# Kernel optimization log

Hardware: AMD Instinct MI355X
Metric: run time of the kernel (lower is better)

## Reference

```python
import jax, jax.numpy as jnp
import numpy as np


def _gru(x, w_ih, w_hh, b_ih, b_hh):
    # x: [B, T, D]; torch nn.GRU (batch_first) semantics, h0 = 0
    B = x.shape[0]
    H = w_hh.shape[1]
    def step(h, xt):
        gi = xt @ w_ih.T + b_ih          # [B, 3H]
        gh = h @ w_hh.T + b_hh           # [B, 3H]
        ir, iz, inn = jnp.split(gi, 3, axis=-1)
        hr, hz, hn = jnp.split(gh, 3, axis=-1)
        r = jax.nn.sigmoid(ir + hr)
        z = jax.nn.sigmoid(iz + hz)
        n = jnp.tanh(inn + r * hn)
        h_new = (1.0 - z) * n + z * h
        return h_new, h_new
    h0 = jnp.zeros((B, H), x.dtype)
    _, ys = jax.lax.scan(step, h0, jnp.swapaxes(x, 0, 1))
    return jnp.swapaxes(ys, 0, 1)        # [B, T, H]


def setup_inputs() -> dict:
    key = jax.random.key(0)
    ks = iter(jax.random.split(key, 40))
    def p(shape, scale=0.05):
        return jax.random.normal(next(ks), shape, dtype=jnp.float32) * scale
    B, T, Z, S = 1024, 2, 100, 6
    return {
        "x": p((B, T, Z, S), 1.0),
        # actor: GRU(6 -> 64) + SimpleSubActor(64 -> 512 -> 128 -> 1)
        "a_gru_wih": p((192, 6)), "a_gru_whh": p((192, 64)),
        "a_gru_bih": p((192,)), "a_gru_bhh": p((192,)),
        "a_fc1_w": p((512, 64)), "a_fc1_b": p((512,)),
        "a_fc2_w": p((128, 512)), "a_fc2_b": p((128,)),
        "a_fc3_w": p((1, 128)), "a_fc3_b": p((1,)),
        # critic: GRU(35 -> 32) + SimpleSubCritic(32 -> 512 -> 256 -> 1)
        "c_gru_wih": p((96, 35)), "c_gru_whh": p((96, 32)),
        "c_gru_bih": p((96,)), "c_gru_bhh": p((96,)),
        "c_fc1_w": p((512, 32)), "c_fc1_b": p((512,)),
        "c_fc2_w": p((256, 512)), "c_fc2_b": p((256,)),
        "c_fc3_w": p((1, 256)), "c_fc3_b": p((1,)),
        # LocalizedModule(35 -> 512 -> 256 -> 1)
        "lm_fc1_w": p((512, 35)), "lm_fc1_b": p((512,)),
        "lm_fc2_w": p((256, 512)), "lm_fc2_b": p((256,)),
        "lm_fc3_w": p((1, 256)), "lm_fc3_b": p((1,)),
    }


def reference(x, a_gru_wih, a_gru_whh, a_gru_bih, a_gru_bhh,
              a_fc1_w, a_fc1_b, a_fc2_w, a_fc2_b, a_fc3_w, a_fc3_b,
              c_gru_wih, c_gru_whh, c_gru_bih, c_gru_bhh,
              c_fc1_w, c_fc1_b, c_fc2_w, c_fc2_b, c_fc3_w, c_fc3_b,
              lm_fc1_w, lm_fc1_b, lm_fc2_w, lm_fc2_b, lm_fc3_w, lm_fc3_b):
    B, T, Z, S = x.shape
    # ---- SimpleActor: same GRU+MLP shared across zones -> batch zones ----
    # torch: a[i] from x[:, :, i]; torch.stack(a) -> [Z, B, T, 1], then .view(-1, T, Z)
    xz = jnp.transpose(x, (2, 0, 1, 3)).reshape(Z * B, T, S)   # zones-major
    sx = _gru(xz, a_gru_wih, a_gru_whh, a_gru_bih, a_gru_bhh)  # [Z*B, T, 64]
    h = jax.nn.relu(sx @ a_fc1_w.T + a_fc1_b)
    h = jax.nn.relu(h @ a_fc2_w.T + a_fc2_b)
    sa = h @ a_fc3_w.T + a_fc3_b                               # [Z*B, T, 1]
    p = sa.reshape(-1, T, Z)                                   # faithful view(-1, t, nzones)
    # ---- concat action onto state ----
    xc = jnp.concatenate([x, p.reshape(-1, T, Z, 1)], axis=-1)  # [B, T, Z, 7]
    # ---- SimpleCritic: f/q lists reset each iter -> only zone i=99 survives ----
    # neighbors of 99: (99, 89, 100->zeros, 109->zeros, 98)
    zeros = jnp.zeros_like(xc[:, :, Z - 1])
    xi = jnp.concatenate([xc[:, :, 99], xc[:, :, 89], zeros, zeros, xc[:, :, 98]], axis=2)  # [B, T, 35]
    # LocalizedModule on last timestep
    hf = jax.nn.relu(xi[:, -1, :] @ lm_fc1_w.T + lm_fc1_b)
    hf = jax.nn.relu(hf @ lm_fc2_w.T + lm_fc2_b)
    f = hf @ lm_fc3_w.T + lm_fc3_b                             # [B, 1]
    # critic GRU + SimpleSubCritic (it keeps only last timestep)
    xq = _gru(xi, c_gru_wih, c_gru_whh, c_gru_bih, c_gru_bhh)  # [B, T, 32]
    hq = jax.nn.relu(xq[:, -1, :] @ c_fc1_w.T + c_fc1_b)
    hq = jax.nn.relu(hq @ c_fc2_w.T + c_fc2_b)
    qz = hq @ c_fc3_w.T + c_fc3_b                              # [B, 1]
    q = jnp.sum(f + qz, axis=1)                                # [B]
    return p[:, -1], q.reshape(-1, 1)
```

## Files before the change

### kernel.cpp

```cpp
#include <hip/hip_runtime.h>
#include <hip/hip_bf16.h>

#define NB 1024
#define NT 2
#define NZ 100
#define NS 6
#define NSEQ (NZ*NB)

typedef short short8 __attribute__((ext_vector_type(8)));
typedef float floatx4 __attribute__((ext_vector_type(4)));
typedef unsigned int uint2v __attribute__((ext_vector_type(2)));

__device__ __forceinline__ float sigm(float v)     { return 1.0f/(1.0f + __expf(-v)); }
__device__ __forceinline__ float tanhfast(float v) { float t = __expf(2.0f*v); return 1.0f - 2.0f/(t + 1.0f); }
__device__ __forceinline__ unsigned short f2bf(float f) {
    __hip_bfloat16 h = __float2bfloat16(f);
    return *reinterpret_cast<unsigned short*>(&h);
}
__device__ __forceinline__ float bf2f(unsigned short u) {
    __hip_bfloat16 h; *reinterpret_cast<unsigned short*>(&h) = u;
    return __bfloat162float(h);
}

#define WS_WIHB   819200
#define WS_WHHB   (WS_WIHB + 192*32*2)
#define WS_W1B    (WS_WHHB + 192*64*2)
#define WS_W2B    (WS_W1B + 512*64*2)
#define WS_L1WB   (WS_W2B + 128*512*2)
#define WS_L2WB   (WS_L1WB + 512*64*2)
#define WS_CF1WB  (WS_L2WB + 256*512*2)
#define WS_CF2WB  (WS_CF1WB + 512*32*2)
#define WS_CWIHB  (WS_CF2WB + 256*512*2)
#define WS_CWHHB  (WS_CWIHB + 96*64*2)

#define PREP_N (116736 + 32768 + 131072 + 16384 + 131072 + 6144 + 3072)

__global__ __launch_bounds__(256)
void prep_kernel(const float* __restrict__ wih, const float* __restrict__ whh,
                 const float* __restrict__ w1,  const float* __restrict__ w2,
                 const float* __restrict__ l1w, const float* __restrict__ l2w,
                 const float* __restrict__ cf1w, const float* __restrict__ cf2w,
                 const float* __restrict__ cwih, const float* __restrict__ cwhh,
                 unsigned short* wihb, unsigned short* whhb,
                 unsigned short* w1b,  unsigned short* w2b,
                 unsigned short* l1wb, unsigned short* l2wb,
                 unsigned short* cf1wb, unsigned short* cf2wb,
                 unsigned short* cwihb, unsigned short* cwhhb)
{
    int e = blockIdx.x*256 + threadIdx.x;
    if (e < 6144) {
        int g = e >> 5, k = e & 31;
        wihb[e] = f2bf(k < 6 ? wih[g*6 + k] : 0.0f);
    } else if (e < 18432) {
        int i = e - 6144;  whhb[i] = f2bf(whh[i]);
    } else if (e < 51200) {
        int i = e - 18432; w1b[i] = f2bf(w1[i]);
    } else if (e < 116736) {
        int i = e - 51200; w2b[i] = f2bf(w2[i]);
    } else if (e < 149504) {
        int i = e - 116736; int o = i >> 6, k = i & 63;
        l1wb[i] = f2bf(k < 35 ? l1w[o*35 + k] : 0.0f);
    } else if (e < 280576) {
        int i = e - 149504; l2wb[i] = f2bf(l2w[i]);
    } else if (e < 296960) {
        int i = e - 280576; cf1wb[i] = f2bf(cf1w[i]);
    } else if (e < 428032) {
        int i = e - 296960; cf2wb[i] = f2bf(cf2w[i]);
    } else if (e < 434176) {
        int i = e - 428032; int o = i >> 6, k = i & 63;
        cwihb[i] = f2bf(k < 35 ? cwih[o*35 + k] : 0.0f);
    } else if (e < PREP_N) {
        int i = e - 434176; cwhhb[i] = f2bf(cwhh[i]);
    }
}

__device__ __forceinline__ short8 ldsfrag(const char* base, int rowstride, int r, int k0) {
    int byte = r*rowstride + k0*2;
    byte ^= ((r & 7) << 4);
    return *reinterpret_cast<const short8*>(base + byte);
}

__global__ __launch_bounds__(512, 4)
void actor_mfma(const float* __restrict__ x,
                const unsigned short* __restrict__ wihb, const unsigned short* __restrict__ whhb,
                const float* __restrict__ bih, const float* __restrict__ bhh,
                const unsigned short* __restrict__ w1b, const float* __restrict__ b1,
                const unsigned short* __restrict__ w2b, const float* __restrict__ b2,
                const float* __restrict__ w3, const float* __restrict__ b3,
                float* __restrict__ sa, float* __restrict__ out0)
{
    __shared__ __align__(16) char smem[73728];
    char*  sxb  = smem;
    float* fc3p = (float*)smem;
    char*  h1b  = smem + 8192;
    char*  xpad = smem + 8192;
    char*  h0b  = smem + 24576;

    const int tid  = threadIdx.x;
    const int wv   = tid >> 6;
    const int lane = tid & 63;
    const int r16  = lane & 15;
    const int g4   = lane >> 4;
    const int ft   = wv & 3;
    const int sq   = wv >> 2;
    const int s0   = blockIdx.x * 32;
    const int zz   = s0 >> 10;
    const int b0   = s0 & 1023;

    for (int e = tid; e < 1024; e += 512) {
        int row = e >> 4, j = e & 15;
        int t = row >> 5, sl = row & 31;
        unsigned int lo = 0, hi = 0;
        if (j < 2) {
            const float* xp = x + (((b0 + sl)*NT + t)*NZ + zz)*NS;
            int c0 = j*4;
            float v0 = xp[c0], v1 = xp[c0+1];
            float v2 = (c0+2 < 6) ? xp[c0+2] : 0.0f;
            float v3 = (c0+3 < 6) ? xp[c0+3] : 0.0f;
            lo = (unsigned int)f2bf(v0) | ((unsigned int)f2bf(v1) << 16);
            hi = (unsigned int)f2bf(v2) | ((unsigned int)f2bf(v3) << 16);
        }
        int byte = row*128 + j*8; byte ^= ((row & 7) << 4);
        uint2v vv = {lo, hi};
        *reinterpret_cast<uint2v*>(xpad + byte) = vv;
    }

    const int fb = ft*16 + g4*4;
    const floatx4 bihR = *reinterpret_cast<const floatx4*>(bih + fb);
    const floatx4 bihZ = *reinterpret_cast<const floatx4*>(bih + 64 + fb);
    const floatx4 bihN = *reinterpret_cast<const floatx4*>(bih + 128 + fb);
    const floatx4 bhhR = *reinterpret_cast<const floatx4*>(bhh + fb);
    const floatx4 bhhZ = *reinterpret_cast<const floatx4*>(bhh + 64 + fb);
    const floatx4 bhhN = *reinterpret_cast<const floatx4*>(bhh + 128 + fb);
    __syncthreads();

    floatx4 h0;
    {
        short8 bx = ldsfrag(xpad, 128, sq*16 + r16, g4*8);
        const short8 aR = *reinterpret_cast<const short8*>(wihb + ((ft     )*16 + r16)*32 + g4*8);
        const short8 aZ = *reinterpret_cast<const short8*>(wihb + ((ft +  4)*16 + r16)*32 + g4*8);
        const short8 aN = *reinterpret_cast<const short8*>(wihb + ((ft +  8)*16 + r16)*32 + g4*8);
        floatx4 gR = {0,0,0,0}, gZ = {0,0,0,0}, gN = {0,0,0,0};
        gR = __builtin_amdgcn_mfma_f32_16x16x32_bf16(aR, bx, gR, 0, 0, 0);
        gZ = __builtin_amdgcn_mfma_f32_16x16x32_bf16(aZ, bx, gZ, 0, 0, 0);
        gN = __builtin_amdgcn_mfma_f32_16x16x32_bf16(aN, bx, gN, 0, 0, 0);
        #pragma unroll
        for (int q = 0; q < 4; ++q) {
            float r = sigm(gR[q] + bihR[q] + bhhR[q]);
            float z = sigm(gZ[q] + bihZ[q] + bhhZ[q]);
            float n = tanhfast(gN[q] + bihN[q] + r*bhhN[q]);
            h0[q] = (1.0f - z)*n;
        }
        unsigned int lo = (unsigned int)f2bf(h0[0]) | ((unsigned int)f2bf(h0[1]) << 16);
        unsigned int hi = (unsigned int)f2bf(h0[2]) | ((unsigned int)f2bf(h0[3]) << 16);
        uint2v vv = {lo, hi};
        int seq = sq*16 + r16;
        int b1a = seq*128 + fb*2; b1a ^= ((seq & 7) << 4);
        *reinterpret_cast<uint2v*>(h0b + b1a) = vv;
        *reinterpret_cast<uint2v*>(sxb + b1a) = vv;
    }

    floatx4 gR1 = {0,0,0,0}, gZ1 = {0,0,0,0}, gN1 = {0,0,0,0};
    {
        short8 bx = ldsfrag(xpad, 128, 32 + sq*16 + r16, g4*8);
        const short8 aR = *reinterpret_cast<const short8*>(wihb + ((ft     )*16 + r16)*32 + g4*8);
        const short8 aZ = *reinterpret_cast<const short8*>(wihb + ((ft +  4)*16 + r16)*32 + g4*8);
        const short8 aN = *reinterpret_cast<const short8*>(wihb + ((ft +  8)*16 + r16)*32 + g4*8);
        gR1 = __builtin_amdgcn_mfma_f32_16x16x32_bf16(aR, bx, gR1, 0, 0, 0);
        gZ1 = __builtin_amdgcn_mfma_f32_16x16x32_bf16(aZ, bx, gZ1, 0, 0, 0);
        gN1 = __builtin_amdgcn_mfma_f32_16x16x32_bf16(aN, bx, gN1, 0, 0, 0);
    }
    __syncthreads();

    {
        short8 bh0 = ldsfrag(h0b, 128, sq*16 + r16, g4*8);
        short8 bh1 = ldsfrag(h0b, 128, sq*16 + r16, 32 + g4*8);
        floatx4 hR = {0,0,0,0}, hZ = {0,0,0,0}, hN = {0,0,0,0};
        #pragma unroll
        for (int p = 0; p < 2; ++p) {
            short8 bh = p ? bh1 : bh0;
            const short8 aR = *reinterpret_cast<const short8*>(whhb + ((ft     )*16 + r16)*64 + p*32 + g4*8);
            const short8 aZ = *reinterpret_cast<const short8*>(whhb + ((ft +  4)*16 + r16)*64 + p*32 + g4*8);
            const short8 aN = *reinterpret_cast<const short8*>(whhb + ((ft +  8)*16 + r16)*64 + p*32 + g4*8);
            hR = __builtin_amdgcn_mfma_f32_16x16x32_bf16(aR, bh, hR, 0, 0, 0);
            hZ = __builtin_amdgcn_mfma_f32_16x16x32_bf16(aZ, bh, hZ, 0, 0, 0);
            hN = __builtin_amdgcn_mfma_f32_16x16x32_bf16(aN, bh, hN, 0, 0, 0);
        }
        floatx4 hn;
        #pragma unroll
        for (int q = 0; q < 4; ++q) {
            float r = sigm(gR1[q] + bihR[q] + hR[q] + bhhR[q]);
            float z = sigm(gZ1[q] + bihZ[q] + hZ[q] + bhhZ[q]);
            float n = tanhfast(gN1[q] + bihN[q] + r*(hN[q] + bhhN[q]));
            hn[q] = (1.0f - z)*n + z*h0[q];
        }
        unsigned int lo = (unsigned int)f2bf(hn[0]) | ((unsigned int)f2bf(hn[1]) << 16);
        unsigned int hi = (unsigned int)f2bf(hn[2]) | ((unsigned int)f2bf(hn[3]) << 16);
        uint2v vv = {lo, hi};
        int row = 32 + sq*16 + r16;
        int ba = row*128 + fb*2; ba ^= ((row & 7) << 4);
        *reinterpret_cast<uint2v*>(sxb + ba) = vv;
    }
    __syncthreads();

    {
        short8 bf[4][2];
        #pragma unroll
        for (int rt = 0; rt < 4; ++rt) {
            bf[rt][0] = ldsfrag(sxb, 128, rt*16 + r16, g4*8);
            bf[rt][1] = ldsfrag(sxb, 128, rt*16 + r16, 32 + g4*8);
        }
        #pragma unroll
        for (int j = 0; j < 4; ++j) {
            int mt = wv*4 + j;
            const short8 a0 = *reinterpret_cast<const short8*>(w1b + (mt*16 + r16)*64 + g4*8);
            const short8 a1 = *reinterpret_cast<const short8*>(w1b + (mt*16 + r16)*64 + 32 + g4*8);
            const floatx4 bias = *reinterpret_cast<const floatx4*>(b1 + mt*16 + g4*4);
            #pragma unroll
            for (int rt = 0; rt < 4; ++rt) {
                floatx4 acc = bias;
                acc = __builtin_amdgcn_mfma_f32_16x16x32_bf16(a0, bf[rt][0], acc, 0, 0, 0);
                acc = __builtin_amdgcn_mfma_f32_16x16x32_bf16(a1, bf[rt][1], acc, 0, 0, 0);
                unsigned int lo = (unsigned int)f2bf(fmaxf(acc[0],0.f)) | ((unsigned int)f2bf(fmaxf(acc[1],0.f)) << 16);
                unsigned int hi = (unsigned int)f2bf(fmaxf(acc[2],0.f)) | ((unsigned int)f2bf(fmaxf(acc[3],0.f)) << 16);
                int row = rt*16 + r16;
                int byte = row*1024 + (mt*16 + g4*4)*2; byte ^= ((row & 7) << 4);
                uint2v vv = {lo, hi};
                *reinterpret_cast<uint2v*>(h1b + byte) = vv;
            }
        }
    }
    __syncthreads();

    {
        floatx4 acc[4];
        const floatx4 bias = *reinterpret_cast<const floatx4*>(b2 + wv*16 + g4*4);
        #pragma unroll
        for (int rt = 0; rt < 4; ++rt) acc[rt] = bias;
        const unsigned short* wp = w2b + (wv*16 + r16)*512 + g4*8;
        for (int ks = 0; ks < 16; ++ks) {
            const short8 a = *reinterpret_cast<const short8*>(wp + ks*32);
            #pragma unroll
            for (int rt = 0; rt < 4; ++rt) {
                short8 bb = ldsfrag(h1b, 1024, rt*16 + r16, ks*32 + g4*8);
                acc[rt] = __builtin_amdgcn_mfma_f32_16x16x32_bf16(a, bb, acc[rt], 0, 0, 0);
            }
        }
        const floatx4 w3v = *reinterpret_cast<const floatx4*>(w3 + wv*16 + g4*4);
        #pragma unroll
        for (int rt = 0; rt < 4; ++rt) {
            float p = fmaxf(acc[rt][0],0.f)*w3v[0] + fmaxf(acc[rt][1],0.f)*w3v[1]
                    + fmaxf(acc[rt][2],0.f)*w3v[2] + fmaxf(acc[rt][3],0.f)*w3v[3];
            p += __shfl_xor(p, 16);
            p += __shfl_xor(p, 32);
            if (g4 == 0) fc3p[wv*64 + rt*16 + r16] = p;
        }
    }
    __syncthreads();

    if (tid < 64) {
        float v = b3[0];
        #pragma unroll
        for (int w = 0; w < 8; ++w) v += fc3p[w*64 + tid];
        int t = tid >> 5, sl = tid & 31;
        int gseq = s0 + sl;
        int i = gseq*2 + t;
        sa[i] = v;
        int m = i % 200;
        if (m >= 100) out0[(i/200)*NZ + (m - 100)] = v;
    }
}

__global__ __launch_bounds__(512)
void critic_mfma(const float* __restrict__ x, const float* __restrict__ sa,
                 const unsigned short* __restrict__ cwihb, const unsigned short* __restrict__ cwhhb,
                 const float* __restrict__ cbih, const float* __restrict__ cbhh,
                 const unsigned short* __restrict__ cf1wb, const float* __restrict__ cf1b,
                 const unsigned short* __restrict__ cf2wb, const float* __restrict__ cf2b,
                 const float* __restrict__ cf3w, const float* __restrict__ cf3b,
                 const unsigned short* __restrict__ l1wb, const float* __restrict__ l1b,
                 const unsigned short* __restrict__ l2wb, const float* __restrict__ l2b,
                 const float* __restrict__ l3w, const float* __restrict__ l3b,
                 float* __restrict__ outq)
{
    __shared__ __align__(16) char smem[25600];
    char*  xib = smem;
    char*  h1b = smem + 4096;
    char*  h0b = smem + 20480;
    char*  hqb = smem + 22528;
    float* fp  = (float*)(smem + 24576);
    float* qp  = (float*)(smem + 25088);

    const int tid  = threadIdx.x;
    const int wv   = tid >> 6;
    const int lane = tid & 63;
    const int r16  = lane & 15;
    const int g4   = lane >> 4;
    const int b0   = blockIdx.x * 16;

    for (int e = tid; e < 2048; e += 512) {
        int trow = e >> 6, k = e & 63;
        int t = trow >> 4, row = trow & 15;
        int b = b0 + row;
        float v = 0.0f;
        if (k < 35) {
            int slot = k / 7, s = k - slot*7;
            int nb = (slot==0)?99:((slot==1)?89:((slot==4)?98:-1));
            if (nb >= 0) v = (s < 6) ? x[((b*NT + t)*NZ + nb)*NS + s]
                                     : sa[b*200 + t*100 + nb];
        }
        int byte = trow*128 + k*2; byte ^= ((trow & 7) << 4);
        *reinterpret_cast<unsigned short*>(xib + byte) = f2bf(v);
    }
    __syncthreads();

    {
        short8 bx0 = ldsfrag(xib, 128, 16 + r16, g4*8);
        short8 bx1 = ldsfrag(xib, 128, 16 + r16, 32 + g4*8);
        #pragma unroll
        for (int j = 0; j < 4; ++j) {
            int mt = wv*4 + j;
            const short8 a0 = *reinterpret_cast<const short8*>(l1wb + (mt*16 + r16)*64 + g4*8);
            const short8 a1 = *reinterpret_cast<const short8*>(l1wb + (mt*16 + r16)*64 + 32 + g4*8);
            floatx4 acc = *reinterpret_cast<const floatx4*>(l1b + mt*16 + g4*4);
            acc = __builtin_amdgcn_mfma_f32_16x16x32_bf16(a0, bx0, acc, 0, 0, 0);
            acc = __builtin_amdgcn_mfma_f32_16x16x32_bf16(a1, bx1, acc, 0, 0, 0);
            unsigned int lo = (unsigned int)f2bf(fmaxf(acc[0],0.f)) | ((unsigned int)f2bf(fmaxf(acc[1],0.f)) << 16);
            unsigned int hi = (unsigned int)f2bf(fmaxf(acc[2],0.f)) | ((unsigned int)f2bf(fmaxf(acc[3],0.f)) << 16);
            int byte = r16*1024 + (mt*16 + g4*4)*2; byte ^= ((r16 & 7) << 4);
            uint2v vv = {lo, hi};
            *reinterpret_cast<uint2v*>(h1b + byte) = vv;
        }
    }
    __syncthreads();

    {
        int mt0 = wv*2, mt1 = wv*2 + 1;
        floatx4 acc0 = *reinterpret_cast<const floatx4*>(l2b + mt0*16 + g4*4);
        floatx4 acc1 = *reinterpret_cast<const floatx4*>(l2b + mt1*16 + g4*4);
        const unsigned short* wp0 = l2wb + (mt0*16 + r16)*512 + g4*8;
        const unsigned short* wp1 = l2wb + (mt1*16 + r16)*512 + g4*8;
        for (int ks = 0; ks < 16; ++ks) {
            short8 bb = ldsfrag(h1b, 1024, r16, ks*32 + g4*8);
            const short8 a0 = *reinterpret_cast<const short8*>(wp0 + ks*32);
            const short8 a1 = *reinterpret_cast<const short8*>(wp1 + ks*32);
            acc0 = __builtin_amdgcn_mfma_f32_16x16x32_bf16(a0, bb, acc0, 0, 0, 0);
            acc1 = __builtin_amdgcn_mfma_f32_16x16x32_bf16(a1, bb, acc1, 0, 0, 0);
        }
        const floatx4 w0 = *reinterpret_cast<const floatx4*>(l3w + mt0*16 + g4*4);
        const floatx4 w1 = *reinterpret_cast<const floatx4*>(l3w + mt1*16 + g4*4);
        float p = fmaxf(acc0[0],0.f)*w0[0] + fmaxf(acc0[1],0.f)*w0[1]
                + fmaxf(acc0[2],0.f)*w0[2] + fmaxf(acc0[3],0.f)*w0[3]
                + fmaxf(acc1[0],0.f)*w1[0] + fmaxf(acc1[1],0.f)*w1[1]
                + fmaxf(acc1[2],0.f)*w1[2] + fmaxf(acc1[3],0.f)*w1[3];
        p += __shfl_xor(p, 16);
        p += __shfl_xor(p, 32);
        if (g4 == 0) fp[wv*16 + r16] = p;
    }
    __syncthreads();

    floatx4 h0r = {0,0,0,0};
    floatx4 gR1 = {0,0,0,0}, gZ1 = {0,0,0,0}, gN1 = {0,0,0,0};
    floatx4 bihR, bihZ, bihN, bhhR, bhhZ, bhhN;
    if (wv < 2) {
        const int hf = wv;
        const int fb = hf*16 + g4*4;
        bihR = *reinterpret_cast<const floatx4*>(cbih + fb);
        bihZ = *reinterpret_cast<const floatx4*>(cbih + 32 + fb);
        bihN = *reinterpret_cast<const floatx4*>(cbih + 64 + fb);
        bhhR = *reinterpret_cast<const floatx4*>(cbhh + fb);
        bhhZ = *reinterpret_cast<const floatx4*>(cbhh + 32 + fb);
        bhhN = *reinterpret_cast<const floatx4*>(cbhh + 64 + fb);
        short8 bx0 = ldsfrag(xib, 128, r16, g4*8);
        short8 bx1 = ldsfrag(xib, 128, r16, 32 + g4*8);
        short8 cx0 = ldsfrag(xib, 128, 16 + r16, g4*8);
        short8 cx1 = ldsfrag(xib, 128, 16 + r16, 32 + g4*8);
        floatx4 gR0 = {0,0,0,0}, gZ0 = {0,0,0,0}, gN0 = {0,0,0,0};
        #pragma unroll
        for (int p = 0; p < 2; ++p) {
            const short8 aR = *reinterpret_cast<const short8*>(cwihb + ((hf    )*16 + r16)*64 + p*32 + g4*8);
            const short8 aZ = *reinterpret_cast<const short8*>(cwihb + ((2+hf  )*16 + r16)*64 + p*32 + g4*8);
            const short8 aN = *reinterpret_cast<const short8*>(cwihb + ((4+hf  )*16 + r16)*64 + p*32 + g4*8);
            short8 b0f = p ? bx1 : bx0;
            short8 b1f = p ? cx1 : cx0;
            gR0 = __builtin_amdgcn_mfma_f32_16x16x32_bf16(aR, b0f, gR0, 0, 0, 0);
            gZ0 = __builtin_amdgcn_mfma_f32_16x16x32_bf16(aZ, b0f, gZ0, 0, 0, 0);
            gN0 = __builtin_amdgcn_mfma_f32_16x16x32_bf16(aN, b0f, gN0, 0, 0, 0);
            gR1 = __builtin_amdgcn_mfma_f32_16x16x32_bf16(aR, b1f, gR1, 0, 0, 0);
            gZ1 = __builtin_amdgcn_mfma_f32_16x16x32_bf16(aZ, b1f, gZ1, 0, 0, 0);
            gN1 = __builtin_amdgcn_mfma_f32_16x16x32_bf16(aN, b1f, gN1, 0, 0, 0);
        }
        #pragma unroll
        for (int q = 0; q < 4; ++q) {
            float r = sigm(gR0[q] + bihR[q] + bhhR[q]);
            float z = sigm(gZ0[q] + bihZ[q] + bhhZ[q]);
            float n = tanhfast(gN0[q] + bihN[q] + r*bhhN[q]);
            h0r[q] = (1.0f - z)*n;
        }
        unsigned int lo = (unsigned int)f2bf(h0r[0]) | ((unsigned int)f2bf(h0r[1]) << 16);
        unsigned int hi = (unsigned int)f2bf(h0r[2]) | ((unsigned int)f2bf(h0r[3]) << 16);
        uint2v vv = {lo, hi};
        int byte = r16*128 + fb*2; byte ^= ((r16 & 7) << 4);
        *reinterpret_cast<uint2v*>(h0b + byte) = vv;
    }
    __syncthreads();
    if (wv < 2) {
        const int hf = wv;
        const int fb = hf*16 + g4*4;
        short8 bh = ldsfrag(h0b, 128, r16, g4*8);
        const short8 aR = *reinterpret_cast<const short8*>(cwhhb + ((hf    )*16 + r16)*32 + g4*8);
        const short8 aZ = *reinterpret_cast<const short8*>(cwhhb + ((2+hf  )*16 + r16)*32 + g4*8);
        const short8 aN = *reinterpret_cast<const short8*>(cwhhb + ((4+hf  )*16 + r16)*32 + g4*8);
        floatx4 hR = {0,0,0,0}, hZ = {0,0,0,0}, hN = {0,0,0,0};
        hR = __builtin_amdgcn_mfma_f32_16x16x32_bf16(aR, bh, hR, 0, 0, 0);
        hZ = __builtin_amdgcn_mfma_f32_16x16x32_bf16(aZ, bh, hZ, 0, 0, 0);
        hN = __builtin_amdgcn_mfma_f32_16x16x32_bf16(aN, bh, hN, 0, 0, 0);
        floatx4 hn;
        #pragma unroll
        for (int q = 0; q < 4; ++q) {
            float r = sigm(gR1[q] + bihR[q] + hR[q] + bhhR[q]);
            float z = sigm(gZ1[q] + bihZ[q] + hZ[q] + bhhZ[q]);
            float n = tanhfast(gN1[q] + bihN[q] + r*(hN[q] + bhhN[q]));
            hn[q] = (1.0f - z)*n + z*h0r[q];
        }
        unsigned int lo = (unsigned int)f2bf(hn[0]) | ((unsigned int)f2bf(hn[1]) << 16);
        unsigned int hi = (unsigned int)f2bf(hn[2]) | ((unsigned int)f2bf(hn[3]) << 16);
        uint2v vv = {lo, hi};
        int byte = r16*128 + fb*2; byte ^= ((r16 & 7) << 4);
        *reinterpret_cast<uint2v*>(hqb + byte) = vv;
    }
    __syncthreads();

    {
        short8 bq = ldsfrag(hqb, 128, r16, g4*8);
        #pragma unroll
        for (int j = 0; j < 4; ++j) {
            int mt = wv*4 + j;
            const short8 a = *reinterpret_cast<const short8*>(cf1wb + (mt*16 + r16)*32 + g4*8);
            floatx4 acc = *reinterpret_cast<const floatx4*>(cf1b + mt*16 + g4*4);
            acc = __builtin_amdgcn_mfma_f32_16x16x32_bf16(a, bq, acc, 0, 0, 0);
            unsigned int lo = (unsigned int)f2bf(fmaxf(acc[0],0.f)) | ((unsigned int)f2bf(fmaxf(acc[1],0.f)) << 16);
            unsigned int hi = (unsigned int)f2bf(fmaxf(acc[2],0.f)) | ((unsigned int)f2bf(fmaxf(acc[3],0.f)) << 16);
            int byte = r16*1024 + (mt*16 + g4*4)*2; byte ^= ((r16 & 7) << 4);
            uint2v vv = {lo, hi};
            *reinterpret_cast<uint2v*>(h1b + byte) = vv;
        }
    }
    __syncthreads();

    {
        int mt0 = wv*2, mt1 = wv*2 + 1;
        floatx4 acc0 = *reinterpret_cast<const floatx4*>(cf2b + mt0*16 + g4*4);
        floatx4 acc1 = *reinterpret_cast<const floatx4*>(cf2b + mt1*16 + g4*4);
        const unsigned short* wp0 = cf2wb + (mt0*16 + r16)*512 + g4*8;
        const unsigned short* wp1 = cf2wb + (mt1*16 + r16)*512 + g4*8;
        for (int ks = 0; ks < 16; ++ks) {
            short8 bb = ldsfrag(h1b, 1024, r16, ks*32 + g4*8);
            const short8 a0 = *reinterpret_cast<const short8*>(wp0 + ks*32);
            const short8 a1 = *reinterpret_cast<const short8*>(wp1 + ks*32);
            acc0 = __builtin_amdgcn_mfma_f32_16x16x32_bf16(a0, bb, acc0, 0, 0, 0);
            acc1 = __builtin_amdgcn_mfma_f32_16x16x32_bf16(a1, bb, acc1, 0, 0, 0);
        }
        const floatx4 w0 = *reinterpret_cast<const floatx4*>(cf3w + mt0*16 + g4*4);
        const floatx4 w1 = *reinterpret_cast<const floatx4*>(cf3w + mt1*16 + g4*4);
        float p = fmaxf(acc0[0],0.f)*w0[0] + fmaxf(acc0[1],0.f)*w0[1]
                + fmaxf(acc0[2],0.f)*w0[2] + fmaxf(acc0[3],0.f)*w0[3]
                + fmaxf(acc1[0],0.f)*w1[0] + fmaxf(acc1[1],0.f)*w1[1]
                + fmaxf(acc1[2],0.f)*w1[2] + fmaxf(acc1[3],0.f)*w1[3];
        p += __shfl_xor(p, 16);
        p += __shfl_xor(p, 32);
        if (g4 == 0) qp[wv*16 + r16] = p;
    }
    __syncthreads();

    if (tid < 16) {
        float f = l3b[0], qz = cf3b[0];
        #pragma unroll
        for (int w = 0; w < 8; ++w) { f += fp[w*16 + tid]; qz += qp[w*16 + tid]; }
        outq[b0 + tid] = f + qz;
    }
}

extern "C" void kernel_launch(void* const* d_in, const int* in_sizes, int n_in,
                              void* d_out, int out_size, void* d_ws, size_t ws_size,
                              hipStream_t stream)
{
    (void)in_sizes; (void)n_in; (void)out_size; (void)ws_size;
    const float* x     = (const float*)d_in[0];
    const float* a_wih = (const float*)d_in[1];
    const float* a_whh = (const float*)d_in[2];
    const float* a_bih = (const float*)d_in[3];
    const float* a_bhh = (const float*)d_in[4];
    const float* a1w   = (const float*)d_in[5];
    const float* a1b   = (const float*)d_in[6];
    const float* a2w   = (const float*)d_in[7];
    const float* a2b   = (const float*)d_in[8];
    const float* a3w   = (const float*)d_in[9];
    const float* a3b   = (const float*)d_in[10];
    const float* cwih  = (const float*)d_in[11];
    const float* cwhh  = (const float*)d_in[12];
    const float* cbih  = (const float*)d_in[13];
    const float* cbhh  = (const float*)d_in[14];
    const float* cf1w  = (const float*)d_in[15];
    const float* cf1b  = (const float*)d_in[16];
    const float* cf2w  = (const float*)d_in[17];
    const float* cf2b  = (const float*)d_in[18];
    const float* cf3w  = (const float*)d_in[19];
    const float* cf3b  = (const float*)d_in[20];
    const float* l1w   = (const float*)d_in[21];
    const float* l1b   = (const float*)d_in[22];
    const float* l2w   = (const float*)d_in[23];
    const float* l2b   = (const float*)d_in[24];
    const float* l3w   = (const float*)d_in[25];
    const float* l3b   = (const float*)d_in[26];

    float* sa = (float*)d_ws;
    unsigned short* wihb  = (unsigned short*)((char*)d_ws + WS_WIHB);
    unsigned short* whhb  = (unsigned short*)((char*)d_ws + WS_WHHB);
    unsigned short* w1b   = (unsigned short*)((char*)d_ws + WS_W1B);
    unsigned short* w2b   = (unsigned short*)((char*)d_ws + WS_W2B);
    unsigned short* l1wb  = (unsigned short*)((char*)d_ws + WS_L1WB);
    unsigned short* l2wb  = (unsigned short*)((char*)d_ws + WS_L2WB);
    unsigned short* cf1wb = (unsigned short*)((char*)d_ws + WS_CF1WB);
    unsigned short* cf2wb = (unsigned short*)((char*)d_ws + WS_CF2WB);
    unsigned short* cwihb = (unsigned short*)((char*)d_ws + WS_CWIHB);
    unsigned short* cwhhb = (unsigned short*)((char*)d_ws + WS_CWHHB);
    float* out0 = (float*)d_out;
    float* outq = (float*)d_out + NB*NZ;

    hipLaunchKernelGGL(prep_kernel, dim3((PREP_N + 255)/256), dim3(256), 0, stream,
                       a_wih, a_whh, a1w, a2w, l1w, l2w, cf1w, cf2w, cwih, cwhh,
                       wihb, whhb, w1b, w2b, l1wb, l2wb, cf1wb, cf2wb, cwihb, cwhhb);
    hipLaunchKernelGGL(actor_mfma, dim3(NSEQ/32), dim3(512), 0, stream,
                       x, wihb, whhb, a_bih, a_bhh, w1b, a1b, w2b, a2b, a3w, a3b, sa, out0);
    hipLaunchKernelGGL(critic_mfma, dim3(NB/16), dim3(512), 0, stream,
                       x, sa, cwihb, cwhhb, cbih, cbhh, cf1wb, cf1b, cf2wb, cf2b, cf3w, cf3b,
                       l1wb, l1b, l2wb, l2b, l3w, l3b, outq);
}
```

Baseline: 145.1 us.

## Split actor fc1/fc2 into two K-halves to halve LDS and raise occupancy

The actor kernel's 512-wide hidden layer is now computed in two halves of 256. Each half goes into a smaller LDS buffer and is accumulated into the fc2 result before the buffer is reused. This cuts shared memory from 72KB to 40KB per block and raises the launch-bounds minimum to 8 blocks per CU, aiming for more resident waves to hide latency. In exchange it adds an extra barrier pair per half and re-reads the sxb fragments, and the tighter register budget may cause spills.

```diff
diff --git a/kernel.cpp b/kernel.cpp
--- a/kernel.cpp
+++ b/kernel.cpp
@@ -16,10 +16,6 @@
 __device__ __forceinline__ unsigned short f2bf(float f) {
     __hip_bfloat16 h = __float2bfloat16(f);
     return *reinterpret_cast<unsigned short*>(&h);
-}
-__device__ __forceinline__ float bf2f(unsigned short u) {
-    __hip_bfloat16 h; *reinterpret_cast<unsigned short*>(&h) = u;
-    return __bfloat162float(h);
 }
 
 #define WS_WIHB   819200
@@ -80,7 +76,7 @@
     return *reinterpret_cast<const short8*>(base + byte);
 }
 
-__global__ __launch_bounds__(512, 4)
+__global__ __launch_bounds__(512, 8)
 void actor_mfma(const float* __restrict__ x,
                 const unsigned short* __restrict__ wihb, const unsigned short* __restrict__ whhb,
                 const float* __restrict__ bih, const float* __restrict__ bhh,
@@ -89,12 +85,12 @@
                 const float* __restrict__ w3, const float* __restrict__ b3,
                 float* __restrict__ sa, float* __restrict__ out0)
 {
-    __shared__ __align__(16) char smem[73728];
+    __shared__ __align__(16) char smem[40960];
     char*  sxb  = smem;
     float* fc3p = (float*)smem;
     char*  h1b  = smem + 8192;
     char*  xpad = smem + 8192;
-    char*  h0b  = smem + 24576;
+    char*  h0b  = smem + 16384;
 
     const int tid  = threadIdx.x;
     const int wv   = tid >> 6;
@@ -203,49 +199,61 @@
     }
     __syncthreads();
 
-    {
-        short8 bf[4][2];
-        #pragma unroll
-        for (int rt = 0; rt < 4; ++rt) {
-            bf[rt][0] = ldsfrag(sxb, 128, rt*16 + r16, g4*8);
-            bf[rt][1] = ldsfrag(sxb, 128, rt*16 + r16, 32 + g4*8);
-        }
-        #pragma unroll
-        for (int j = 0; j < 4; ++j) {
-            int mt = wv*4 + j;
-            const short8 a0 = *reinterpret_cast<const short8*>(w1b + (mt*16 + r16)*64 + g4*8);
-            const short8 a1 = *reinterpret_cast<const short8*>(w1b + (mt*16 + r16)*64 + 32 + g4*8);
-            const floatx4 bias = *reinterpret_cast<const floatx4*>(b1 + mt*16 + g4*4);
+    floatx4 acc[4];
+    {
+        const floatx4 bias2 = *reinterpret_cast<const floatx4*>(b2 + wv*16 + g4*4);
+        #pragma unroll
+        for (int rt = 0; rt < 4; ++rt) acc[rt] = bias2;
+    }
+
+    #pragma unroll
+    for (int h = 0; h < 2; ++h) {
+        {
+            short8 bfr[4][2];
             #pragma unroll
             for (int rt = 0; rt < 4; ++rt) {
-                floatx4 acc = bias;
-                acc = __builtin_amdgcn_mfma_f32_16x16x32_bf16(a0, bf[rt][0], acc, 0, 0, 0);
-                acc = __builtin_amdgcn_mfma_f32_16x16x32_bf16(a1, bf[rt][1], acc, 0, 0, 0);
-                unsigned int lo = (unsigned int)f2bf(fmaxf(acc[0],0.f)) | ((unsigned int)f2bf(fmaxf(acc[1],0.f)) << 16);
-                unsigned int hi = (unsigned int)f2bf(fmaxf(acc[2],0.f)) | ((unsigned int)f2bf(fmaxf(acc[3],0.f)) << 16);
-                int row = rt*16 + r16;
-                int byte = row*1024 + (mt*16 + g4*4)*2; byte ^= ((row & 7) << 4);
-                uint2v vv = {lo, hi};
-                *reinterpret_cast<uint2v*>(h1b + byte) = vv;
+                bfr[rt][0] = ldsfrag(sxb, 128, rt*16 + r16, g4*8);
+                bfr[rt][1] = ldsfrag(sxb, 128, rt*16 + r16, 32 + g4*8);
             }
-        }
-    }
-    __syncthreads();
-
-    {
-        floatx4 acc[4];
-        const floatx4 bias = *reinterpret_cast<const floatx4*>(b2 + wv*16 + g4*4);
-        #pragma unroll
-        for (int rt = 0; rt < 4; ++rt) acc[rt] = bias;
-        const unsigned short* wp = w2b + (wv*16 + r16)*512 + g4*8;
-        for (int ks = 0; ks < 16; ++ks) {
-            const short8 a = *reinterpret_cast<const short8*>(wp + ks*32);
             #pragma unroll
-            for (int rt = 0; rt < 4; ++rt) {
-                short8 bb = ldsfrag(h1b, 1024, rt*16 + r16, ks*32 + g4*8);
-                acc[rt] = __builtin_amdgcn_mfma_f32_16x16x32_bf16(a, bb, acc[rt], 0, 0, 0);
+            for (int j = 0; j < 2; ++j) {
+                int mtg = h*16 + wv*2 + j;
+                int mtl = wv*2 + j;
+                const short8 a0 = *reinterpret_cast<const short8*>(w1b + (mtg*16 + r16)*64 + g4*8);
+                const short8 a1 = *reinterpret_cast<const short8*>(w1b + (mtg*16 + r16)*64 + 32 + g4*8);
+                const floatx4 bias = *reinterpret_cast<const floatx4*>(b1 + mtg*16 + g4*4);
+                #pragma unroll
+                for (int rt = 0; rt < 4; ++rt) {
+                    floatx4 a = bias;
+                    a = __builtin_amdgcn_mfma_f32_16x16x32_bf16(a0, bfr[rt][0], a, 0, 0, 0);
+                    a = __builtin_amdgcn_mfma_f32_16x16x32_bf16(a1, bfr[rt][1], a, 0, 0, 0);
+                    unsigned int lo = (unsigned int)f2bf(fmaxf(a[0],0.f)) | ((unsigned int)f2bf(fmaxf(a[1],0.f)) << 16);
+                    unsigned int hi = (unsigned int)f2bf(fmaxf(a[2],0.f)) | ((unsigned int)f2bf(fmaxf(a[3],0.f)) << 16);
+                    int row = rt*16 + r16;
+                    int byte = row*512 + (mtl*16 + g4*4)*2; byte ^= ((row & 7) << 4);
+                    uint2v vv = {lo, hi};
+                    *reinterpret_cast<uint2v*>(h1b + byte) = vv;
+                }
             }
         }
+        __syncthreads();
+
+        {
+            const unsigned short* wp = w2b + (wv*16 + r16)*512 + h*256 + g4*8;
+            #pragma unroll
+            for (int ks = 0; ks < 8; ++ks) {
+                const short8 a = *reinterpret_cast<const short8*>(wp + ks*32);
+                #pragma unroll
+                for (int rt = 0; rt < 4; ++rt) {
+                    short8 bb = ldsfrag(h1b, 512, rt*16 + r16, ks*32 + g4*8);
+                    acc[rt] = __builtin_amdgcn_mfma_f32_16x16x32_bf16(a, bb, acc[rt], 0, 0, 0);
+                }
+            }
+        }
+        __syncthreads();
+    }
+
+    {
         const floatx4 w3v = *reinterpret_cast<const floatx4*>(w3 + wv*16 + g4*4);
         #pragma unroll
         for (int rt = 0; rt < 4; ++rt) {
```

After: 285.0 us. +96.5%, slower.
